# Kernel tuning notes

Measured on AMD Instinct MI355X. Metric: run time of the kernel, lower is better.

Reference implementation:

```python
import jax, jax.numpy as jnp
import numpy as np

DECAY = 0.99
EPSILON = 1e-05
BETA = 0.25  # vq_commitment_beta


def setup_inputs() -> dict:
    key = jax.random.key(0)
    k1, k2, k3, k4 = jax.random.split(key, 4)
    N, dim, K = 32768, 512, 8192
    init_range = 1.0 / np.sqrt(dim)
    emb_w = jax.random.uniform(k3, (K, 2 * dim), dtype=jnp.float32,
                               minval=-init_range, maxval=init_range)
    return {
        "z_real": jax.random.normal(k1, (N, dim), dtype=jnp.float32),
        "z_imag": jax.random.normal(k2, (N, dim), dtype=jnp.float32),
        "emb_w": emb_w,
        "ema_cluster_size": jnp.zeros((K,), dtype=jnp.float32),
        "ema_w": emb_w.copy(),
    }


def reference(z_real, z_imag, emb_w, ema_cluster_size, ema_w):
    N, dim = z_real.shape
    K = emb_w.shape[0]
    z_flat = jnp.concatenate([z_real, z_imag], axis=-1)  # [N, 2*dim]

    # squared euclidean distances [N, K]
    x_sq = jnp.sum(z_flat * z_flat, axis=1, keepdims=True)
    y_sq = jnp.sum(emb_w * emb_w, axis=1)
    d = jnp.maximum(x_sq + y_sq - 2.0 * (z_flat @ emb_w.T), 0.0)
    indices = jnp.argmin(d, axis=-1)  # [N]
    z_q = emb_w[indices]              # [N, 2*dim]

    # EMA codebook update (training-mode buffer math, no grads)
    n_total = jnp.zeros((K,), z_flat.dtype).at[indices].add(1.0)
    new_cluster_size = ema_cluster_size * DECAY + (1.0 - DECAY) * n_total
    cs = new_cluster_size + EPSILON
    cs = cs + (cs < 1.0).astype(cs.dtype)
    dw = jnp.zeros((K, 2 * dim), z_flat.dtype).at[indices].add(z_flat)  # encodings.T @ z_flat
    new_ema_w = ema_w * DECAY + (1.0 - DECAY) * dw
    new_w = jnp.clip(new_ema_w / cs[:, None], -5.0, 5.0)

    loss_sample = BETA * jnp.mean((z_q - z_flat) ** 2, axis=-1)  # [N]

    # straight-through (forward value == z_q)
    z_q_st = z_flat + jax.lax.stop_gradient(z_q - z_flat)

    probs = n_total / N
    norm_entropy = -jnp.sum(probs * jnp.log(probs + 1e-10)) / np.log(float(K))

    z_q_r = z_q_st[..., :dim]
    z_q_i = z_q_st[..., dim:]
    return (z_q_r, z_q_i, loss_sample, indices, norm_entropy,
            new_w, new_cluster_size, new_ema_w)
```

## Files before the change

### kernel.cpp

```cpp
#include <hip/hip_runtime.h>
#include <hip/hip_bf16.h>

#define NROWS 32768
#define DIM   512
#define D2    1024
#define KCODE 8192
#define DECAYF 0.99f
#define OMD    0.01f
#define MARGIN 0.30f
#define CANDCAP 16
#define ZMAX 6.0f
#define IRANGE 0.04419417382415922f

typedef __attribute__((ext_vector_type(4))) float f32x4;
typedef __attribute__((ext_vector_type(4))) int   v4i;
typedef __attribute__((ext_vector_type(16))) int  i32x16;

#define WS_EMB8    0u
#define WS_YSQ     8388608u
#define WS_NINT    8421376u
#define WS_ENT     8454144u
#define WS_CCOUNT  8454160u
#define WS_CAND    8585232u
#define WS_FIDX    10682384u
#define WS_OFF     10813456u
#define WS_CUR     10846224u
#define WS_ROWLIST 10878992u

#define OUT_ZQR  0
#define OUT_ZQI  16777216
#define OUT_LOSS 33554432
#define OUT_IDX  33587200
#define OUT_ENT  33619968
#define OUT_NEWW 33619969
#define OUT_NCS  42008577
#define OUT_NEMA 42016769

__device__ __forceinline__ float wredf(float v) {
    #pragma unroll
    for (int o = 32; o > 0; o >>= 1) v += __shfl_down(v, o, 64);
    return v;
}

__device__ __forceinline__ double wredd(double v) {
    #pragma unroll
    for (int o = 32; o > 0; o >>= 1) v += __shfl_down(v, o, 64);
    return __shfl(v, 0, 64);
}

__device__ __forceinline__ double ulp32_of(double v) {
    return scalbn(1.0, ilogb(v) - 23);
}

__device__ __forceinline__ void gload_lds16(const void* g, void* l) {
    __builtin_amdgcn_global_load_lds(
        (const __attribute__((address_space(1))) unsigned int*)(g),
        (__attribute__((address_space(3))) unsigned int*)(l), 16, 0, 0);
}

__device__ __forceinline__ int q4(float4 v, float s) {
    int a = (int)rintf(fminf(fmaxf(v.x * s, -127.f), 127.f));
    int b = (int)rintf(fminf(fmaxf(v.y * s, -127.f), 127.f));
    int c = (int)rintf(fminf(fmaxf(v.z * s, -127.f), 127.f));
    int d = (int)rintf(fminf(fmaxf(v.w * s, -127.f), 127.f));
    return (a & 255) | ((b & 255) << 8) | ((c & 255) << 16) | ((d & 255) << 24);
}

__global__ __launch_bounds__(256) void prep_emb(const float* __restrict__ emb,
                                                char* __restrict__ emb8,
                                                float* __restrict__ ysq) {
    int wave = threadIdx.x >> 6, lane = threadIdx.x & 63;
    int k = blockIdx.x * 4 + wave;
    const float4* src = (const float4*)(emb + (size_t)k * D2);
    v4i* dst = (v4i*)(emb8 + (size_t)k * D2);
    const float es = 127.0f / IRANGE;
    float s = 0.f;
    float4 v0 = src[lane * 4 + 0];
    float4 v1 = src[lane * 4 + 1];
    float4 v2 = src[lane * 4 + 2];
    float4 v3 = src[lane * 4 + 3];
    s += v0.x*v0.x + v0.y*v0.y + v0.z*v0.z + v0.w*v0.w;
    s += v1.x*v1.x + v1.y*v1.y + v1.z*v1.z + v1.w*v1.w;
    s += v2.x*v2.x + v2.y*v2.y + v2.z*v2.z + v2.w*v2.w;
    s += v3.x*v3.x + v3.y*v3.y + v3.z*v3.z + v3.w*v3.w;
    v4i pk; pk[0] = q4(v0, es); pk[1] = q4(v1, es); pk[2] = q4(v2, es); pk[3] = q4(v3, es);
    dst[lane] = pk;
    s = wredf(s);
    if (lane == 0) ysq[k] = s;
}

__global__ __launch_bounds__(256, 2) void argmin_gemm(
    const float* __restrict__ zr, const float* __restrict__ zi,
    const char* __restrict__ emb8, const float* __restrict__ ysq,
    long long* __restrict__ pairs)
{
    __shared__ char bufs[2][16384];
    const int tid  = threadIdx.x;
    const int wave = tid >> 6, lane = tid & 63;
    const int colc = lane & 31;
    const int hh   = lane >> 5;
    const int rowblk = blockIdx.x >> 1;
    const int slice  = blockIdx.x & 1;

    const int arow = rowblk * 128 + wave * 32 + colc;
    const float zs = 127.0f / ZMAX;
    const float* zrp = zr + (size_t)arow * 512 + hh * 16;
    const float* zip = zi + (size_t)arow * 512 + hh * 16;
    v4i afrag[32];
    #pragma unroll
    for (int ft = 0; ft < 16; ++ft) {
        const float4* p = (const float4*)(zrp + ft * 32);
        v4i a; a[0] = q4(p[0], zs); a[1] = q4(p[1], zs); a[2] = q4(p[2], zs); a[3] = q4(p[3], zs);
        afrag[ft] = a;
    }
    #pragma unroll
    for (int ft = 0; ft < 16; ++ft) {
        const float4* p = (const float4*)(zip + ft * 32);
        v4i a; a[0] = q4(p[0], zs); a[1] = q4(p[1], zs); a[2] = q4(p[2], zs); a[3] = q4(p[3], zs);
        afrag[16 + ft] = a;
    }

    float tv0[16], tv1[16];
    int cpk[16];
    #pragma unroll
    for (int g = 0; g < 16; ++g) { tv0[g] = 3.4e38f; tv1[g] = 3.4e38f; cpk[g] = 0; }

    const char* gslice = emb8 + (size_t)slice * 4096 * 1024;
    const float* yslice = ysq + slice * 4096;

#define STAGE(dstbuf, chunk_, h_) do {                                           \
        const char* gb = gslice + ((size_t)(chunk_) * 32 * 1024 + (size_t)(h_) * 512); \
        _Pragma("unroll")                                                        \
        for (int p = 0; p < 4; ++p) {                                            \
            int s_ = p * 4096 + wave * 1024 + lane * 16;                         \
            int code_ = s_ >> 9;                                                 \
            int c16p_ = (s_ & 511) >> 4;                                         \
            gload_lds16(gb + (size_t)code_ * 1024 + ((c16p_ ^ (code_ & 7)) << 4), \
                        &(dstbuf)[p * 4096 + wave * 1024]);                      \
        }                                                                        \
    } while (0)

    const char* bb0 = &bufs[0][0] + colc * 512;
    const char* bb1 = &bufs[1][0] + colc * 512;
    const int bxor = colc & 7;
    const float sfac = 2.0f * (ZMAX / 127.0f) * (IRANGE / 127.0f);

    STAGE(bufs[0], 0, 0);
    __syncthreads();

    for (int c = 0; c < 128; ++c) {
        STAGE(bufs[1], c, 1);
        i32x16 acc0, acc1;
        #pragma unroll
        for (int g = 0; g < 16; ++g) { acc0[g] = 0; acc1[g] = 0; }
        #pragma unroll
        for (int kt = 0; kt < 16; kt += 2) {
            v4i b0 = *(const v4i*)(bb0 + ((((kt    ) * 2 + hh) ^ bxor) << 4));
            v4i b1 = *(const v4i*)(bb0 + ((((kt + 1) * 2 + hh) ^ bxor) << 4));
            acc0 = __builtin_amdgcn_mfma_i32_32x32x32_i8(afrag[kt],     b0, acc0, 0, 0, 0);
            acc1 = __builtin_amdgcn_mfma_i32_32x32x32_i8(afrag[kt + 1], b1, acc1, 0, 0, 0);
        }
        __syncthreads();

        if (c + 1 < 128) STAGE(bufs[0], c + 1, 0);
        #pragma unroll
        for (int kt = 0; kt < 16; kt += 2) {
            v4i b0 = *(const v4i*)(bb1 + ((((kt    ) * 2 + hh) ^ bxor) << 4));
            v4i b1 = *(const v4i*)(bb1 + ((((kt + 1) * 2 + hh) ^ bxor) << 4));
            acc0 = __builtin_amdgcn_mfma_i32_32x32x32_i8(afrag[16 + kt],     b0, acc0, 0, 0, 0);
            acc1 = __builtin_amdgcn_mfma_i32_32x32x32_i8(afrag[16 + kt + 1], b1, acc1, 0, 0, 0);
        }
        float ysv = yslice[c * 32 + colc];
        #pragma unroll
        for (int g = 0; g < 16; ++g) {
            float fdot = (float)(acc0[g] + acc1[g]);
            float sc = fmaf(-sfac, fdot, ysv);
            if (sc < tv1[g]) {
                bool b0 = sc < tv0[g];
                int cp = cpk[g];
                cpk[g] = b0 ? (((cp & 0xFF) << 8) | c) : ((cp & 0xFF) | (c << 8));
                float ov0 = tv0[g];
                tv1[g] = b0 ? ov0 : sc;
                tv0[g] = b0 ? sc : ov0;
            }
        }
        __syncthreads();
    }
#undef STAGE

    #pragma unroll
    for (int g = 0; g < 16; ++g) {
        int rloc = (g & 3) + 8 * (g >> 2) + 4 * hh;
        int rowg = rowblk * 128 + wave * 32 + rloc;
        size_t base = (size_t)rowg * 128 + slice * 64 + colc * 2;
        int cp = cpk[g];
        int code0 = slice * 4096 + (cp & 0xFF) * 32 + colc;
        int code1 = slice * 4096 + ((cp >> 8) & 0xFF) * 32 + colc;
        pairs[base + 0] = ((long long)(unsigned)code0 << 32) | (unsigned)__float_as_uint(tv0[g]);
        pairs[base + 1] = ((long long)(unsigned)code1 << 32) | (unsigned)__float_as_uint(tv1[g]);
    }
}

__global__ __launch_bounds__(256) void merge_rows(const long long* __restrict__ pairs,
                                                  int* __restrict__ cand,
                                                  int* __restrict__ ccount)
{
    int wave = threadIdx.x >> 6, lane = threadIdx.x & 63;
    int row = blockIdx.x * 4 + wave;
    const long long* pr = pairs + (size_t)row * 128;
    long long p0 = pr[lane];
    long long p1 = pr[64 + lane];
    float v0v = __uint_as_float((unsigned)p0);
    int   i0  = (int)(p0 >> 32);
    float v1v = __uint_as_float((unsigned)p1);
    int   i1  = (int)(p1 >> 32);
    float m = fminf(v0v, v1v);
    #pragma unroll
    for (int o = 32; o > 0; o >>= 1) m = fminf(m, __shfl_xor(m, o, 64));
    float lim = m + MARGIN;
    unsigned long long m0 = __ballot(v0v < lim);
    unsigned long long m1 = __ballot(v1v < lim);
    int t0 = __popcll(m0);
    int cnt = t0 + __popcll(m1);
    if (cnt > CANDCAP) cnt = CANDCAP;
    unsigned long long below = (lane == 63) ? 0xFFFFFFFFFFFFFFFFull >> 1
                                            : ((1ull << lane) - 1);
    if (v0v < lim) {
        int pos = __popcll(m0 & below);
        if (pos < CANDCAP) cand[(size_t)row * CANDCAP + pos] = i0;
    }
    if (v1v < lim) {
        int pos = t0 + __popcll(m1 & below);
        if (pos < CANDCAP) cand[(size_t)row * CANDCAP + pos] = i1;
    }
    if (lane == 0) ccount[row] = cnt;
}

__global__ __launch_bounds__(256) void cleanup(
    const float* __restrict__ zr, const float* __restrict__ zi,
    const float* __restrict__ emb, const int* __restrict__ cand,
    const int* __restrict__ ccount, int* __restrict__ fidx,
    int* __restrict__ nint, float* __restrict__ out)
{
    int wave = threadIdx.x >> 6, lane = threadIdx.x & 63;
    int r = blockIdx.x * 4 + wave;
    int cnt = ccount[r];
    int best = cand[r * CANDCAP];
    if (cnt > 1) {
        float zreg[16];
        double xs = 0.0;
        #pragma unroll
        for (int p = 0; p < 4; ++p) {
            int d4 = p * 64 + lane;
            const float4* zp = (d4 < 128) ? (const float4*)(zr + (size_t)r * 512)
                                          : ((const float4*)(zi + (size_t)r * 512) - 128);
            float4 zv = zp[d4];
            zreg[p * 4 + 0] = zv.x; zreg[p * 4 + 1] = zv.y;
            zreg[p * 4 + 2] = zv.z; zreg[p * 4 + 3] = zv.w;
            xs += (double)zv.x * zv.x + (double)zv.y * zv.y
                + (double)zv.z * zv.z + (double)zv.w * zv.w;
        }
        xs = wredd(xs);
        double uS = ulp32_of(xs);

        double bD = 1e300; int bi = 1 << 30;
        for (int i = 0; i < cnt; ++i) {
            int cdx = cand[r * CANDCAP + i];
            const float4* ep = (const float4*)(emb + (size_t)cdx * 1024);
            double ys = 0.0, tt = 0.0;
            #pragma unroll
            for (int p = 0; p < 4; ++p) {
                float4 ev = ep[p * 64 + lane];
                float p0 = ev.x * ev.x, p1 = ev.y * ev.y, p2 = ev.z * ev.z, p3 = ev.w * ev.w;
                ys += (double)p0 + (double)p1 + (double)p2 + (double)p3;
                tt += (double)zreg[p * 4 + 0] * (double)ev.x
                    + (double)zreg[p * 4 + 1] * (double)ev.y
                    + (double)zreg[p * 4 + 2] * (double)ev.z
                    + (double)zreg[p * 4 + 3] * (double)ev.w;
            }
            ys = wredd(ys);
            tt = wredd(tt);
            float y32 = (float)ys;
            float t32 = (float)tt;
            double dex = xs + ys - 2.0 * tt;
            double ud = ulp32_of(dex);
            double D = rint((double)y32 / uS) * uS - rint(2.0 * (double)t32 / ud) * ud;
            if (D < bD || (D == bD && cdx < bi)) { bD = D; bi = cdx; }
        }
        best = bi;
    }
    if (lane == 0) {
        fidx[r] = best;
        out[OUT_IDX + r] = (float)best;
        atomicAdd(nint + best, 1);
    }
}

__global__ __launch_bounds__(256) void scan_codes(const int* __restrict__ nint,
                                                  int* __restrict__ off,
                                                  int* __restrict__ cur) {
    __shared__ int part[256];
    int tid = threadIdx.x;
    int base = tid * 32;
    int loc[32];
    int s = 0;
    #pragma unroll
    for (int j = 0; j < 32; ++j) { loc[j] = s; s += nint[base + j]; }
    part[tid] = s;
    __syncthreads();
    for (int o = 1; o < 256; o <<= 1) {
        int t = (tid >= o) ? part[tid - o] : 0;
        __syncthreads();
        part[tid] += t;
        __syncthreads();
    }
    int excl = part[tid] - s;
    #pragma unroll
    for (int j = 0; j < 32; ++j) {
        off[base + j] = excl + loc[j];
        cur[base + j] = 0;
    }
}

__global__ __launch_bounds__(256) void fill_rows(const int* __restrict__ fidx,
                                                 const int* __restrict__ off,
                                                 int* __restrict__ cur,
                                                 int* __restrict__ rowlist) {
    int r = blockIdx.x * 256 + threadIdx.x;
    int idx = fidx[r];
    int pos = atomicAdd(cur + idx, 1);
    rowlist[off[idx] + pos] = r;
}

__global__ __launch_bounds__(256) void ema_update(
    const float* __restrict__ zr, const float* __restrict__ zi,
    const float* __restrict__ emaw, const float* __restrict__ emacs,
    const int* __restrict__ nint, const int* __restrict__ off,
    const int* __restrict__ rowlist, float* __restrict__ out,
    float* __restrict__ entacc)
{
    int k = blockIdx.x;
    int tid = threadIdx.x;
    int cnt = nint[k];
    int o0 = off[k];
    float ax = 0.f, ay = 0.f, az = 0.f, aw = 0.f;
    for (int i = 0; i < cnt; ++i) {
        int r = rowlist[o0 + i];
        float4 zv = (tid < 128) ? ((const float4*)(zr + (size_t)r * 512))[tid]
                                : ((const float4*)(zi + (size_t)r * 512))[tid - 128];
        ax += zv.x; ay += zv.y; az += zv.z; aw += zv.w;
    }
    float4 ew = ((const float4*)(emaw + (size_t)k * 1024))[tid];
    float4 nem;
    nem.x = DECAYF * ew.x + OMD * ax;
    nem.y = DECAYF * ew.y + OMD * ay;
    nem.z = DECAYF * ew.z + OMD * az;
    nem.w = DECAYF * ew.w + OMD * aw;
    ((float4*)(out + OUT_NEMA + (size_t)k * 1024))[tid] = nem;
    float ncs = DECAYF * emacs[k] + OMD * (float)cnt;
    float cs = ncs + 1e-5f;
    if (cs < 1.f) cs += 1.f;
    float inv = 1.f / cs;
    float4 w;
    w.x = fminf(fmaxf(nem.x * inv, -5.f), 5.f);
    w.y = fminf(fmaxf(nem.y * inv, -5.f), 5.f);
    w.z = fminf(fmaxf(nem.z * inv, -5.f), 5.f);
    w.w = fminf(fmaxf(nem.w * inv, -5.f), 5.f);
    ((float4*)(out + OUT_NEWW + (size_t)k * 1024))[tid] = w;
    if (tid == 0) {
        out[OUT_NCS + k] = ncs;
        float p = (float)cnt / 32768.f;
        atomicAdd(entacc, -p * logf(p + 1e-10f));
    }
}

__global__ void ent_fin(const float* __restrict__ entacc, float* __restrict__ out) {
    if (threadIdx.x == 0) out[OUT_ENT] = entacc[0] / logf(8192.f);
}

__global__ __launch_bounds__(256) void zq_loss(
    const float* __restrict__ zr, const float* __restrict__ zi,
    const float* __restrict__ emb, const int* __restrict__ fidx, float* __restrict__ out)
{
    int wave = threadIdx.x >> 6, lane = threadIdx.x & 63;
    int r = blockIdx.x * 4 + wave;
    int idx = fidx[r];
    const float4* ep = (const float4*)(emb + (size_t)idx * 1024);
    float acc = 0.f;
    #pragma unroll
    for (int p = 0; p < 4; ++p) {
        int d4 = p * 64 + lane;
        const float4* zp = (d4 < 128) ? (const float4*)(zr + (size_t)r * 512)
                                      : ((const float4*)(zi + (size_t)r * 512) - 128);
        float4 zv = zp[d4];
        float4 ev = ep[d4];
        float dx = ev.x - zv.x; acc += dx * dx;
        float dy = ev.y - zv.y; acc += dy * dy;
        float dz = ev.z - zv.z; acc += dz * dz;
        float dw = ev.w - zv.w; acc += dw * dw;
        float4* op = (d4 < 128) ? (float4*)(out + OUT_ZQR + (size_t)r * 512)
                                : ((float4*)(out + OUT_ZQI + (size_t)r * 512) - 128);
        op[d4] = ev;
    }
    acc = wredf(acc);
    if (lane == 0) out[OUT_LOSS + r] = 0.25f * acc * (1.f / 1024.f);
}

extern "C" void kernel_launch(void* const* d_in, const int* in_sizes, int n_in,
                              void* d_out, int out_size, void* d_ws, size_t ws_size,
                              hipStream_t stream)
{
    const float* zr    = (const float*)d_in[0];
    const float* zi    = (const float*)d_in[1];
    const float* emb   = (const float*)d_in[2];
    const float* emacs = (const float*)d_in[3];
    const float* emaw  = (const float*)d_in[4];
    float* out = (float*)d_out;
    char* ws = (char*)d_ws;

    char*  emb8    = (char*)(ws + WS_EMB8);
    float* ysq     = (float*)(ws + WS_YSQ);
    int*   nint    = (int*)(ws + WS_NINT);
    float* entacc  = (float*)(ws + WS_ENT);
    int*   ccount  = (int*)(ws + WS_CCOUNT);
    int*   cand    = (int*)(ws + WS_CAND);
    int*   fidx    = (int*)(ws + WS_FIDX);
    int*   off     = (int*)(ws + WS_OFF);
    int*   cur     = (int*)(ws + WS_CUR);
    int*   rowlist = (int*)(ws + WS_ROWLIST);
    long long* pairs = (long long*)out;

    hipMemsetAsync(ws + WS_NINT, 0, 32768 + 16, stream);

    prep_emb   <<<2048, 256, 0, stream>>>(emb, emb8, ysq);
    argmin_gemm<<<512,  256, 0, stream>>>(zr, zi, emb8, ysq, pairs);
    merge_rows <<<8192, 256, 0, stream>>>(pairs, cand, ccount);
    cleanup    <<<8192, 256, 0, stream>>>(zr, zi, emb, cand, ccount, fidx, nint, out);
    scan_codes <<<1,    256, 0, stream>>>(nint, off, cur);
    fill_rows  <<<128,  256, 0, stream>>>(fidx, off, cur, rowlist);
    ema_update <<<8192, 256, 0, stream>>>(zr, zi, emaw, emacs, nint, off, rowlist, out, entacc);
    ent_fin    <<<1,    64,  0, stream>>>(entacc, out);
    zq_loss    <<<8192, 256, 0, stream>>>(zr, zi, emb, fidx, out);
}
```

Measured before the change: 603.8 us.

## Pre-transpose int8 codebook into MFMA fragment order and stage full chunks

prep_emb now writes the quantized codebook in a per-32-code chunk layout ordered by MFMA fragment, so every 16-byte lane fragment is contiguous. argmin_gemm stages a whole 32 KB chunk per buffer with plain linear global-to-LDS loads, dropping the XOR swizzle and the half-chunk split. That removes one __syncthreads per chunk and simplifies LDS addressing. The cost is double the LDS use (64 KB per block), which may limit occupancy to the two blocks requested by the launch bounds.

Result: faster. 587.9 us (-2.6%).

```diff
diff --git a/kernel.cpp b/kernel.cpp
--- a/kernel.cpp
+++ b/kernel.cpp
@@ -16,7 +16,7 @@
 typedef __attribute__((ext_vector_type(4))) int   v4i;
 typedef __attribute__((ext_vector_type(16))) int  i32x16;
 
-#define WS_EMB8    0u
+#define WS_EMB8T   0u
 #define WS_YSQ     8388608u
 #define WS_NINT    8421376u
 #define WS_ENT     8454144u
@@ -67,12 +67,11 @@
 }
 
 __global__ __launch_bounds__(256) void prep_emb(const float* __restrict__ emb,
-                                                char* __restrict__ emb8,
+                                                char* __restrict__ emb8t,
                                                 float* __restrict__ ysq) {
     int wave = threadIdx.x >> 6, lane = threadIdx.x & 63;
     int k = blockIdx.x * 4 + wave;
     const float4* src = (const float4*)(emb + (size_t)k * D2);
-    v4i* dst = (v4i*)(emb8 + (size_t)k * D2);
     const float es = 127.0f / IRANGE;
     float s = 0.f;
     float4 v0 = src[lane * 4 + 0];
@@ -84,17 +83,18 @@
     s += v2.x*v2.x + v2.y*v2.y + v2.z*v2.z + v2.w*v2.w;
     s += v3.x*v3.x + v3.y*v3.y + v3.z*v3.z + v3.w*v3.w;
     v4i pk; pk[0] = q4(v0, es); pk[1] = q4(v1, es); pk[2] = q4(v2, es); pk[3] = q4(v3, es);
-    dst[lane] = pk;
+    v4i* dst = (v4i*)(emb8t + (size_t)(k >> 5) * 32768 + (size_t)lane * 512 + (k & 31) * 16);
+    *dst = pk;
     s = wredf(s);
     if (lane == 0) ysq[k] = s;
 }
 
 __global__ __launch_bounds__(256, 2) void argmin_gemm(
     const float* __restrict__ zr, const float* __restrict__ zi,
-    const char* __restrict__ emb8, const float* __restrict__ ysq,
+    const char* __restrict__ emb8t, const float* __restrict__ ysq,
     long long* __restrict__ pairs)
 {
-    __shared__ char bufs[2][16384];
+    __shared__ char bufs[2][32768];
     const int tid  = threadIdx.x;
     const int wave = tid >> 6, lane = tid & 63;
     const int colc = lane & 31;
@@ -125,51 +125,40 @@
     #pragma unroll
     for (int g = 0; g < 16; ++g) { tv0[g] = 3.4e38f; tv1[g] = 3.4e38f; cpk[g] = 0; }
 
-    const char* gslice = emb8 + (size_t)slice * 4096 * 1024;
+    const char* gslice = emb8t + (size_t)slice * 128 * 32768;
     const float* yslice = ysq + slice * 4096;
 
-#define STAGE(dstbuf, chunk_, h_) do {                                           \
-        const char* gb = gslice + ((size_t)(chunk_) * 32 * 1024 + (size_t)(h_) * 512); \
+#define STAGE(dstbuf, chunk_) do {                                               \
+        const char* gb = gslice + (size_t)(chunk_) * 32768 + wave * 8192         \
+                       + (size_t)lane * 16;                                      \
+        char* lb = (dstbuf) + wave * 8192;                                       \
         _Pragma("unroll")                                                        \
-        for (int p = 0; p < 4; ++p) {                                            \
-            int s_ = p * 4096 + wave * 1024 + lane * 16;                         \
-            int code_ = s_ >> 9;                                                 \
-            int c16p_ = (s_ & 511) >> 4;                                         \
-            gload_lds16(gb + (size_t)code_ * 1024 + ((c16p_ ^ (code_ & 7)) << 4), \
-                        &(dstbuf)[p * 4096 + wave * 1024]);                      \
-        }                                                                        \
+        for (int q = 0; q < 8; ++q)                                              \
+            gload_lds16(gb + q * 1024, lb + q * 1024);                           \
     } while (0)
 
-    const char* bb0 = &bufs[0][0] + colc * 512;
-    const char* bb1 = &bufs[1][0] + colc * 512;
-    const int bxor = colc & 7;
     const float sfac = 2.0f * (ZMAX / 127.0f) * (IRANGE / 127.0f);
-
-    STAGE(bufs[0], 0, 0);
+    const int boff = colc * 16 + hh * 512;
+
+    STAGE(bufs[0], 0);
     __syncthreads();
 
     for (int c = 0; c < 128; ++c) {
-        STAGE(bufs[1], c, 1);
+        const int cur = c & 1;
+        if (c + 1 < 128) STAGE(bufs[cur ^ 1], c + 1);
+
+        const char* bb = &bufs[cur][0] + boff;
         i32x16 acc0, acc1;
         #pragma unroll
         for (int g = 0; g < 16; ++g) { acc0[g] = 0; acc1[g] = 0; }
         #pragma unroll
-        for (int kt = 0; kt < 16; kt += 2) {
-            v4i b0 = *(const v4i*)(bb0 + ((((kt    ) * 2 + hh) ^ bxor) << 4));
-            v4i b1 = *(const v4i*)(bb0 + ((((kt + 1) * 2 + hh) ^ bxor) << 4));
-            acc0 = __builtin_amdgcn_mfma_i32_32x32x32_i8(afrag[kt],     b0, acc0, 0, 0, 0);
-            acc1 = __builtin_amdgcn_mfma_i32_32x32x32_i8(afrag[kt + 1], b1, acc1, 0, 0, 0);
+        for (int m = 0; m < 32; m += 2) {
+            v4i b0 = *(const v4i*)(bb + (m    ) * 1024);
+            v4i b1 = *(const v4i*)(bb + (m + 1) * 1024);
+            acc0 = __builtin_amdgcn_mfma_i32_32x32x32_i8(afrag[m],     b0, acc0, 0, 0, 0);
+            acc1 = __builtin_amdgcn_mfma_i32_32x32x32_i8(afrag[m + 1], b1, acc1, 0, 0, 0);
         }
-        __syncthreads();
-
-        if (c + 1 < 128) STAGE(bufs[0], c + 1, 0);
-        #pragma unroll
-        for (int kt = 0; kt < 16; kt += 2) {
-            v4i b0 = *(const v4i*)(bb1 + ((((kt    ) * 2 + hh) ^ bxor) << 4));
-            v4i b1 = *(const v4i*)(bb1 + ((((kt + 1) * 2 + hh) ^ bxor) << 4));
-            acc0 = __builtin_amdgcn_mfma_i32_32x32x32_i8(afrag[16 + kt],     b0, acc0, 0, 0, 0);
-            acc1 = __builtin_amdgcn_mfma_i32_32x32x32_i8(afrag[16 + kt + 1], b1, acc1, 0, 0, 0);
-        }
+
         float ysv = yslice[c * 32 + colc];
         #pragma unroll
         for (int g = 0; g < 16; ++g) {
@@ -418,7 +407,7 @@
     float* out = (float*)d_out;
     char* ws = (char*)d_ws;
 
-    char*  emb8    = (char*)(ws + WS_EMB8);
+    char*  emb8t   = (char*)(ws + WS_EMB8T);
     float* ysq     = (float*)(ws + WS_YSQ);
     int*   nint    = (int*)(ws + WS_NINT);
     float* entacc  = (float*)(ws + WS_ENT);
@@ -432,8 +421,8 @@
 
     hipMemsetAsync(ws + WS_NINT, 0, 32768 + 16, stream);
 
-    prep_emb   <<<2048, 256, 0, stream>>>(emb, emb8, ysq);
-    argmin_gemm<<<512,  256, 0, stream>>>(zr, zi, emb8, ysq, pairs);
+    prep_emb   <<<2048, 256, 0, stream>>>(emb, emb8t, ysq);
+    argmin_gemm<<<512,  256, 0, stream>>>(zr, zi, emb8t, ysq, pairs);
     merge_rows <<<8192, 256, 0, stream>>>(pairs, cand, ccount);
     cleanup    <<<8192, 256, 0, stream>>>(zr, zi, emb, cand, ccount, fidx, nint, out);
     scan_codes <<<1,    256, 0, stream>>>(nint, off, cur);
```
